# Optimization experiments

Measured on AMD Instinct MI355X. Metric: run time of the kernel, lower is better.

Reference implementation:

```python
import jax, jax.numpy as jnp
import numpy as np

N = 10000   # num nodes
E = 160000  # num edges (avg degree 16)
B = 8       # batch dim carried on node state
D = 64      # hidden_size


def setup_inputs() -> dict:
    key = jax.random.key(0)
    k1, k2, k3, k4, k5, k6 = jax.random.split(key, 6)
    state = jax.random.normal(k1, (N, B, D), jnp.float32)
    feature = jax.random.normal(k2, (N, 32), jnp.float32)  # unused by GAT math, kept for call signature
    weight = jax.random.normal(k3, (2 * D, D), jnp.float32) * 0.05
    src = jax.random.randint(k4, (E,), 0, N, jnp.int32)
    dst = jax.random.randint(k5, (E,), 0, N, jnp.int32)
    dist = jax.random.uniform(k6, (E, 1), jnp.float32)
    return dict(state=state, feature=feature, weight=weight, src=src, dst=dst, dist=dist)


def reference(state, feature, weight, src, dst, dist):
    # --- msg_edge: gather src/dst node states per edge ---
    src_state = state[src]                 # [E,B,D]
    dst_state = state[dst]                 # [E,B,D]
    es = jnp.concatenate([src_state, dst_state], axis=-1)          # [E,B,2D]
    alpha = jax.nn.leaky_relu(jnp.einsum('ebk,kd->ebd', es, weight),
                              negative_slope=0.2)                  # tf.nn.leaky_relu alpha=0.2
    alpha = alpha * dist[:, :, None]       # dist [E,1] broadcast to [E,1,1]

    # --- msg_reduce: segment softmax over incoming edges of each dst node ---
    amax = jax.ops.segment_max(alpha, dst, num_segments=N)         # [N,B,D]
    ex = jnp.exp(alpha - amax[dst])                                # stable exp
    denom = jax.ops.segment_sum(ex, dst, num_segments=N)           # [N,B,D]
    attn = ex / denom[dst]                                         # [E,B,D]

    # weighted sum of src states scattered back to dst nodes, then relu
    new_state = jax.nn.relu(jax.ops.segment_sum(attn * src_state, dst, num_segments=N))
    return new_state
```

## Files before the change

kernel.cpp:

```cpp
#include <hip/hip_runtime.h>
#include <hip/hip_fp16.h>
#include <math.h>

#define N_NODES 10000
#define N_EDGES 160000
#define B_ 8
#define D_ 64
#define BD 512
#define ROWS 80000
#define SLICE 640000
#define CAP 48
#define CAPR 56

typedef _Float16 f16x8 __attribute__((ext_vector_type(8)));
typedef float f32x4 __attribute__((ext_vector_type(4)));
typedef float f4v __attribute__((ext_vector_type(4)));
typedef unsigned int u32;

union HU { _Float16 f; unsigned short u; };
union HC { u32 u; __half2 h; };

__global__ void __launch_bounds__(256, 4) prep_kernel(
    const int* __restrict__ src, const int* __restrict__ dst,
    const float* __restrict__ dist, int* __restrict__ counts, u32* __restrict__ bucket,
    const float* __restrict__ state, const float* __restrict__ weight,
    u32* __restrict__ G, __half* __restrict__ Pd) {
    __shared__ _Float16 At[64 * 72];
    __shared__ char smemB[128 * 72 * 2];
    _Float16* Bt = (_Float16*)smemB;
    unsigned short* Ps2 = (unsigned short*)smemB;
    unsigned short* Ps  = (unsigned short*)(smemB + 8704);
    int bid = blockIdx.x;
    int tid = threadIdx.x;

    int s_e, d_e; float di_e;
    bool do_edge = tid < 128;
    if (do_edge) {
        int e = bid * 128 + tid;
        s_e = src[e];
        d_e = dst[e];
        di_e = dist[e];
    }

    int row0 = bid * 64;
    int wave = tid >> 6, lane = tid & 63;
    int quad = lane >> 4, m16 = lane & 15;
    int m_loc = wave * 16 + m16;

    const f4v* st4 = (const f4v*)(state + (size_t)row0 * 64);
    for (int i = tid; i < 1024; i += 256) {
        int r = i >> 4, c4 = (i & 15) << 2;
        f4v v = __builtin_nontemporal_load(&st4[i]);
        union { short4 s; _Float16 h[4]; } u;
        u.h[0] = (_Float16)v[0]; u.h[1] = (_Float16)v[1];
        u.h[2] = (_Float16)v[2]; u.h[3] = (_Float16)v[3];
        *(short4*)&At[r * 72 + c4] = u.s;
    }
    const f4v* w4 = (const f4v*)weight;
    for (int i = tid; i < 2048; i += 256) {
        int r = i >> 4, c4 = (i & 15) << 2;
        f4v v = w4[i];
        int h = r >> 6, k = r & 63;
        int nb = h * 64 + c4;
        Bt[(nb + 0) * 72 + k] = (_Float16)v[0];
        Bt[(nb + 1) * 72 + k] = (_Float16)v[1];
        Bt[(nb + 2) * 72 + k] = (_Float16)v[2];
        Bt[(nb + 3) * 72 + k] = (_Float16)v[3];
    }

    if (do_edge) {
        int pos = atomicAdd(&counts[d_e], 1);
        if (pos < CAP) {
            unsigned short hd = __half_as_ushort(__float2half_rn(di_e * 1.44269504f));
            bucket[d_e * CAPR + pos] = (u32)s_e | ((u32)hd << 16);
        }
    }
    __syncthreads();

    f16x8 bf0[8], bf1[8];
#pragma unroll
    for (int tcol = 0; tcol < 8; tcol++) {
        int n = tcol * 16 + m16;
        bf0[tcol] = *(const f16x8*)&Bt[n * 72 + quad * 8];
        bf1[tcol] = *(const f16x8*)&Bt[n * 72 + 32 + quad * 8];
    }
    f16x8 a0 = *(const f16x8*)&At[m_loc * 72 + quad * 8];
    f16x8 a1 = *(const f16x8*)&At[m_loc * 72 + 32 + quad * 8];
    __syncthreads();

#pragma unroll
    for (int tcol = 0; tcol < 8; tcol++) {
        int n = tcol * 16 + m16;
        f32x4 acc = {0.f, 0.f, 0.f, 0.f};
        acc = __builtin_amdgcn_mfma_f32_16x16x32_f16(a0, bf0[tcol], acc, 0, 0, 0);
        acc = __builtin_amdgcn_mfma_f32_16x16x32_f16(a1, bf1[tcol], acc, 0, 0, 0);
#pragma unroll
        for (int r = 0; r < 4; r++) {
            int ml = wave * 16 + quad * 4 + r;
            unsigned short ph = __half_as_ushort(__float2half_rn(acc[r]));
            if (tcol < 4) Ps2[ml * 68 + n] = ph;
            else          Ps[ml * 64 + (n - 64)] = ph;
        }
    }
    __syncthreads();

    const u32* Ps2w = (const u32*)Ps2;
    const u32* Atw = (const u32*)At;
    for (int i = tid; i < 1024; i += 256) {
        int row = i >> 4, q = i & 15;
        int m = row0 + row;
        size_t base = (size_t)(m & 7) * SLICE + (size_t)(m >> 3) * 64;
        u32 p01 = Ps2w[row * 34 + q * 2];
        u32 p23 = Ps2w[row * 34 + q * 2 + 1];
        u32 x01 = Atw[row * 36 + q * 2];
        u32 x23 = Atw[row * 36 + q * 2 + 1];
        float4 v = make_float4(__uint_as_float(p01), __uint_as_float(p23),
                               __uint_as_float(x01), __uint_as_float(x23));
        *(float4*)&G[base + q * 4] = v;
    }
    for (int i = tid; i < 512; i += 256) {
        int row = i >> 3, seg = i & 7;
        int m = row0 + row;
        size_t base = (size_t)(m & 7) * SLICE + (size_t)(m >> 3) * 64;
        *(float4*)&Pd[base + seg * 8] = *(const float4*)&Ps[row * 64 + seg * 8];
    }
}

__global__ void __launch_bounds__(256) gat_aggregate(
    const u32* __restrict__ G,
    const __half* __restrict__ Pds,
    const int* __restrict__ counts,
    const u32* __restrict__ bucket,
    float* __restrict__ out) {
    int bid = blockIdx.x;
    int b = bid & 7;
    int grp = bid >> 3;
    int wave = threadIdx.x >> 6;
    int lane = threadIdx.x & 63;
    int n0 = (grp << 3) + (wave << 1);
    int n1 = n0 + 1;
    int eidx = lane >> 4;
    int lpart = lane & 15;

    const u32* Gb = G + (size_t)b * SLICE;
    const __half* Pb = Pds + (size_t)b * SLICE;

    int cnt0 = counts[n0]; if (cnt0 > CAP) cnt0 = CAP;
    int cnt1 = counts[n1]; if (cnt1 > CAP) cnt1 = CAP;
    const u32* ep0 = bucket + n0 * CAPR;
    const u32* ep1 = bucket + n1 * CAPR;

    union { double d; __half2 h[2]; } pdu0, pdu1;
    pdu0.d = *(const double*)(Pb + n0 * 64 + lpart * 4);
    pdu1.d = *(const double*)(Pb + n1 * 64 + lpart * 4);

    u32 rA0 = ep0[eidx], rB0 = ep0[4 + eidx];
    u32 rA1 = ep1[eidx], rB1 = ep1[4 + eidx];
    float4 gA0 = *(const float4*)(Gb + (size_t)(rA0 & 0xffffu) * 64 + lpart * 4);
    float4 gB0 = *(const float4*)(Gb + (size_t)(rB0 & 0xffffu) * 64 + lpart * 4);
    float4 gA1 = *(const float4*)(Gb + (size_t)(rA1 & 0xffffu) * 64 + lpart * 4);
    float4 gB1 = *(const float4*)(Gb + (size_t)(rB1 & 0xffffu) * 64 + lpart * 4);
    __half hh;
    hh = __ushort_as_half((unsigned short)(rA0 >> 16)); __half2 dA0 = __halves2half2(hh, hh);
    hh = __ushort_as_half((unsigned short)(rB0 >> 16)); __half2 dB0 = __halves2half2(hh, hh);
    hh = __ushort_as_half((unsigned short)(rA1 >> 16)); __half2 dA1 = __halves2half2(hh, hh);
    hh = __ushort_as_half((unsigned short)(rB1 >> 16)); __half2 dB1 = __halves2half2(hh, hh);

    const __half2 c06 = __float2half2_rn(0.6f);
    const __half2 c04 = __float2half2_rn(0.4f);

    auto edge_body = [&](float4 g, __half2 dd, __half2 pd01, __half2 pd23,
                         __half2& l01, __half2& l23, __half2& o01, __half2& o23) {
        union { float4 f; __half2 h[4]; } gu; gu.f = g;
        __half2 z01 = __hadd2(gu.h[0], pd01);
        __half2 z23 = __hadd2(gu.h[1], pd23);
        HC zz01, zz23, az01, az23;
        zz01.h = z01; zz23.h = z23;
        az01.u = zz01.u & 0x7fff7fffu;
        az23.u = zz23.u & 0x7fff7fffu;
        __half2 lk01 = __hfma2(az01.h, c04, __hmul2(z01, c06));
        __half2 lk23 = __hfma2(az23.h, c04, __hmul2(z23, c06));
        __half2 a01 = __hmul2(lk01, dd);
        __half2 a23 = __hmul2(lk23, dd);
        __half2 e01 = __halves2half2(hexp2(__low2half(a01)), hexp2(__high2half(a01)));
        __half2 e23 = __halves2half2(hexp2(__low2half(a23)), hexp2(__high2half(a23)));
        l01 = __hadd2(l01, e01);
        l23 = __hadd2(l23, e23);
        o01 = __hfma2(e01, gu.h[2], o01);
        o23 = __hfma2(e23, gu.h[3], o23);
    };

    auto run_task = [&](const u32* ep, int cnt, __half2 pd01, __half2 pd23,
                        float4 gA, float4 gB, __half2 dA, __half2 dB,
                        __half2& l01, __half2& l23, __half2& o01, __half2& o23) {
        int padded4 = (cnt + 3) & ~3;
        int full8 = padded4 & ~7;
        if (full8 > 0) {
            int j = 0;
            for (;;) {
                int jn = j + 8;
                bool more = jn < full8;
                float4 gA2, gB2; __half2 dA2, dB2;
                if (more) {
                    u32 rA2 = ep[jn + eidx];
                    u32 rB2 = ep[jn + 4 + eidx];
                    gA2 = *(const float4*)(Gb + (size_t)(rA2 & 0xffffu) * 64 + lpart * 4);
                    gB2 = *(const float4*)(Gb + (size_t)(rB2 & 0xffffu) * 64 + lpart * 4);
                    __half h2a = __ushort_as_half((unsigned short)(rA2 >> 16));
                    __half h2b = __ushort_as_half((unsigned short)(rB2 >> 16));
                    dA2 = __halves2half2(h2a, h2a);
                    dB2 = __halves2half2(h2b, h2b);
                }
                edge_body(gA, dA, pd01, pd23, l01, l23, o01, o23);
                edge_body(gB, dB, pd01, pd23, l01, l23, o01, o23);
                if (!more) break;
                j = jn; gA = gA2; gB = gB2; dA = dA2; dB = dB2;
            }
            if (padded4 > full8) {
                u32 rec = ep[full8 + eidx];
                float4 g = *(const float4*)(Gb + (size_t)(rec & 0xffffu) * 64 + lpart * 4);
                __half hd = __ushort_as_half((unsigned short)(rec >> 16));
                edge_body(g, __halves2half2(hd, hd), pd01, pd23, l01, l23, o01, o23);
            }
        } else if (padded4 > 0) {
            edge_body(gA, dA, pd01, pd23, l01, l23, o01, o23);
        }
    };

    __half2 zero = __float2half2_rn(0.f);
    __half2 l01a = zero, l23a = zero, o01a = zero, o23a = zero;
    __half2 l01b = zero, l23b = zero, o01b = zero, o23b = zero;

    run_task(ep0, cnt0, pdu0.h[0], pdu0.h[1], gA0, gB0, dA0, dB0, l01a, l23a, o01a, o23a);
    run_task(ep1, cnt1, pdu1.h[0], pdu1.h[1], gA1, gB1, dA1, dB1, l01b, l23b, o01b, o23b);

    float4 g0 = *(const float4*)(Gb + lpart * 4);
    union { float4 f; __half2 h[4]; } g0u; g0u.f = g0;

    auto finish = [&](int cnt, __half2& l01, __half2& l23, __half2& o01, __half2& o23) {
        if (cnt <= 0) return;
#pragma unroll
        for (int m = 16; m <= 32; m <<= 1) {
            HC c;
            c.u = (u32)__shfl_xor((int)((HC){.h = l01}).u, m, 64); l01 = __hadd2(l01, c.h);
            c.u = (u32)__shfl_xor((int)((HC){.h = l23}).u, m, 64); l23 = __hadd2(l23, c.h);
            c.u = (u32)__shfl_xor((int)((HC){.h = o01}).u, m, 64); o01 = __hadd2(o01, c.h);
            c.u = (u32)__shfl_xor((int)((HC){.h = o23}).u, m, 64); o23 = __hadd2(o23, c.h);
        }
        int npads = ((cnt + 3) & ~3) - cnt;
        if (npads) {
            __half2 np = __float2half2_rn((float)npads);
            l01 = __hsub2(l01, np);
            l23 = __hsub2(l23, np);
            __half2 nneg = __hneg2(np);
            o01 = __hfma2(nneg, g0u.h[2], o01);
            o23 = __hfma2(nneg, g0u.h[3], o23);
        }
    };
    finish(cnt0, l01a, l23a, o01a, o23a);
    finish(cnt1, l01b, l23b, o01b, o23b);

    if (eidx == 0) {
        auto emit = [&](int n, int cnt, __half2 l01, __half2 l23, __half2 o01, __half2 o23) {
            float4 r;
            if (cnt > 0) {
                float l0 = __low2float(l01), l1 = __high2float(l01);
                float l2 = __low2float(l23), l3 = __high2float(l23);
                float o0 = __low2float(o01), o1 = __high2float(o01);
                float o2 = __low2float(o23), o3 = __high2float(o23);
                r.x = fmaxf(o0 * __builtin_amdgcn_rcpf(l0), 0.f);
                r.y = fmaxf(o1 * __builtin_amdgcn_rcpf(l1), 0.f);
                r.z = fmaxf(o2 * __builtin_amdgcn_rcpf(l2), 0.f);
                r.w = fmaxf(o3 * __builtin_amdgcn_rcpf(l3), 0.f);
            } else {
                r = make_float4(0.f, 0.f, 0.f, 0.f);
            }
            *(float4*)(out + (size_t)n * BD + b * 64 + lpart * 4) = r;
        };
        emit(n0, cnt0, l01a, l23a, o01a, o23a);
        emit(n1, cnt1, l01b, l23b, o01b, o23b);
    }
}

extern "C" void kernel_launch(void* const* d_in, const int* in_sizes, int n_in,
                              void* d_out, int out_size, void* d_ws, size_t ws_size,
                              hipStream_t stream) {
    const float* state  = (const float*)d_in[0];
    const float* weight = (const float*)d_in[2];
    const int*   src    = (const int*)d_in[3];
    const int*   dst    = (const int*)d_in[4];
    const float* dist   = (const float*)d_in[5];

    u32*    G      = (u32*)d_ws;
    __half* Pd     = (__half*)(G + (size_t)8 * SLICE);
    u32*    bucket = (u32*)(Pd + (size_t)8 * SLICE);
    int*    counts = (int*)(bucket + (size_t)N_NODES * CAPR);

    hipMemsetAsync(bucket, 0, ((size_t)N_NODES * CAPR + N_NODES) * sizeof(u32), stream);
    prep_kernel<<<1250, 256, 0, stream>>>(src, dst, dist, counts, bucket,
                                          state, weight, G, Pd);
    gat_aggregate<<<N_NODES, 256, 0, stream>>>(G, Pd, counts, bucket, (float*)d_out);
}
```

Baseline: 136.5 us.

## Use persistent blocks with atomic work queue per batch slice in aggregation

New measurement: 170.3 us. 24.8% more time.

```diff
diff --git a/kernel.cpp b/kernel.cpp
--- a/kernel.cpp
+++ b/kernel.cpp
@@ -7,10 +7,10 @@
 #define B_ 8
 #define D_ 64
 #define BD 512
-#define ROWS 80000
 #define SLICE 640000
 #define CAP 48
 #define CAPR 56
+#define NPAIRS 5000
 
 typedef _Float16 f16x8 __attribute__((ext_vector_type(8)));
 typedef float f32x4 __attribute__((ext_vector_type(4)));
@@ -131,43 +131,23 @@
     const __half* __restrict__ Pds,
     const int* __restrict__ counts,
     const u32* __restrict__ bucket,
+    int* __restrict__ q,
     float* __restrict__ out) {
-    int bid = blockIdx.x;
-    int b = bid & 7;
-    int grp = bid >> 3;
-    int wave = threadIdx.x >> 6;
+    int s = blockIdx.x & 7;
     int lane = threadIdx.x & 63;
-    int n0 = (grp << 3) + (wave << 1);
-    int n1 = n0 + 1;
     int eidx = lane >> 4;
     int lpart = lane & 15;
 
-    const u32* Gb = G + (size_t)b * SLICE;
-    const __half* Pb = Pds + (size_t)b * SLICE;
-
-    int cnt0 = counts[n0]; if (cnt0 > CAP) cnt0 = CAP;
-    int cnt1 = counts[n1]; if (cnt1 > CAP) cnt1 = CAP;
-    const u32* ep0 = bucket + n0 * CAPR;
-    const u32* ep1 = bucket + n1 * CAPR;
-
-    union { double d; __half2 h[2]; } pdu0, pdu1;
-    pdu0.d = *(const double*)(Pb + n0 * 64 + lpart * 4);
-    pdu1.d = *(const double*)(Pb + n1 * 64 + lpart * 4);
-
-    u32 rA0 = ep0[eidx], rB0 = ep0[4 + eidx];
-    u32 rA1 = ep1[eidx], rB1 = ep1[4 + eidx];
-    float4 gA0 = *(const float4*)(Gb + (size_t)(rA0 & 0xffffu) * 64 + lpart * 4);
-    float4 gB0 = *(const float4*)(Gb + (size_t)(rB0 & 0xffffu) * 64 + lpart * 4);
-    float4 gA1 = *(const float4*)(Gb + (size_t)(rA1 & 0xffffu) * 64 + lpart * 4);
-    float4 gB1 = *(const float4*)(Gb + (size_t)(rB1 & 0xffffu) * 64 + lpart * 4);
-    __half hh;
-    hh = __ushort_as_half((unsigned short)(rA0 >> 16)); __half2 dA0 = __halves2half2(hh, hh);
-    hh = __ushort_as_half((unsigned short)(rB0 >> 16)); __half2 dB0 = __halves2half2(hh, hh);
-    hh = __ushort_as_half((unsigned short)(rA1 >> 16)); __half2 dA1 = __halves2half2(hh, hh);
-    hh = __ushort_as_half((unsigned short)(rB1 >> 16)); __half2 dB1 = __halves2half2(hh, hh);
+    const u32* Gb = G + (size_t)s * SLICE;
+    const __half* Pb = Pds + (size_t)s * SLICE;
+    int* qs = q + s * 32;
 
     const __half2 c06 = __float2half2_rn(0.6f);
     const __half2 c04 = __float2half2_rn(0.4f);
+    const __half2 zero = __float2half2_rn(0.f);
+
+    float4 g0 = *(const float4*)(Gb + lpart * 4);
+    union { float4 f; __half2 h[4]; } g0u; g0u.f = g0;
 
     auto edge_body = [&](float4 g, __half2 dd, __half2 pd01, __half2 pd23,
                          __half2& l01, __half2& l23, __half2& o01, __half2& o23) {
@@ -227,16 +207,6 @@
         }
     };
 
-    __half2 zero = __float2half2_rn(0.f);
-    __half2 l01a = zero, l23a = zero, o01a = zero, o23a = zero;
-    __half2 l01b = zero, l23b = zero, o01b = zero, o23b = zero;
-
-    run_task(ep0, cnt0, pdu0.h[0], pdu0.h[1], gA0, gB0, dA0, dB0, l01a, l23a, o01a, o23a);
-    run_task(ep1, cnt1, pdu1.h[0], pdu1.h[1], gA1, gB1, dA1, dB1, l01b, l23b, o01b, o23b);
-
-    float4 g0 = *(const float4*)(Gb + lpart * 4);
-    union { float4 f; __half2 h[4]; } g0u; g0u.f = g0;
-
     auto finish = [&](int cnt, __half2& l01, __half2& l23, __half2& o01, __half2& o23) {
         if (cnt <= 0) return;
 #pragma unroll
@@ -257,28 +227,72 @@
             o23 = __hfma2(nneg, g0u.h[3], o23);
         }
     };
-    finish(cnt0, l01a, l23a, o01a, o23a);
-    finish(cnt1, l01b, l23b, o01b, o23b);
-
-    if (eidx == 0) {
-        auto emit = [&](int n, int cnt, __half2 l01, __half2 l23, __half2 o01, __half2 o23) {
-            float4 r;
-            if (cnt > 0) {
-                float l0 = __low2float(l01), l1 = __high2float(l01);
-                float l2 = __low2float(l23), l3 = __high2float(l23);
-                float o0 = __low2float(o01), o1 = __high2float(o01);
-                float o2 = __low2float(o23), o3 = __high2float(o23);
-                r.x = fmaxf(o0 * __builtin_amdgcn_rcpf(l0), 0.f);
-                r.y = fmaxf(o1 * __builtin_amdgcn_rcpf(l1), 0.f);
-                r.z = fmaxf(o2 * __builtin_amdgcn_rcpf(l2), 0.f);
-                r.w = fmaxf(o3 * __builtin_amdgcn_rcpf(l3), 0.f);
-            } else {
-                r = make_float4(0.f, 0.f, 0.f, 0.f);
-            }
-            *(float4*)(out + (size_t)n * BD + b * 64 + lpart * 4) = r;
-        };
-        emit(n0, cnt0, l01a, l23a, o01a, o23a);
-        emit(n1, cnt1, l01b, l23b, o01b, o23b);
+
+    auto do_pair = [&](int n0) {
+        int n1 = n0 + 1;
+        int2 c01 = *(const int2*)(counts + n0);
+        int cnt0 = c01.x > CAP ? CAP : c01.x;
+        int cnt1 = c01.y > CAP ? CAP : c01.y;
+        const u32* ep0 = bucket + n0 * CAPR;
+        const u32* ep1 = bucket + n1 * CAPR;
+
+        union { double d; __half2 h[2]; } pdu0, pdu1;
+        pdu0.d = *(const double*)(Pb + n0 * 64 + lpart * 4);
+        pdu1.d = *(const double*)(Pb + n1 * 64 + lpart * 4);
+
+        u32 rA0 = ep0[eidx], rB0 = ep0[4 + eidx];
+        u32 rA1 = ep1[eidx], rB1 = ep1[4 + eidx];
+        float4 gA0 = *(const float4*)(Gb + (size_t)(rA0 & 0xffffu) * 64 + lpart * 4);
+        float4 gB0 = *(const float4*)(Gb + (size_t)(rB0 & 0xffffu) * 64 + lpart * 4);
+        float4 gA1 = *(const float4*)(Gb + (size_t)(rA1 & 0xffffu) * 64 + lpart * 4);
+        float4 gB1 = *(const float4*)(Gb + (size_t)(rB1 & 0xffffu) * 64 + lpart * 4);
+        __half hh;
+        hh = __ushort_as_half((unsigned short)(rA0 >> 16)); __half2 dA0 = __halves2half2(hh, hh);
+        hh = __ushort_as_half((unsigned short)(rB0 >> 16)); __half2 dB0 = __halves2half2(hh, hh);
+        hh = __ushort_as_half((unsigned short)(rA1 >> 16)); __half2 dA1 = __halves2half2(hh, hh);
+        hh = __ushort_as_half((unsigned short)(rB1 >> 16)); __half2 dB1 = __halves2half2(hh, hh);
+
+        __half2 l01a = zero, l23a = zero, o01a = zero, o23a = zero;
+        __half2 l01b = zero, l23b = zero, o01b = zero, o23b = zero;
+
+        run_task(ep0, cnt0, pdu0.h[0], pdu0.h[1], gA0, gB0, dA0, dB0, l01a, l23a, o01a, o23a);
+        run_task(ep1, cnt1, pdu1.h[0], pdu1.h[1], gA1, gB1, dA1, dB1, l01b, l23b, o01b, o23b);
+
+        finish(cnt0, l01a, l23a, o01a, o23a);
+        finish(cnt1, l01b, l23b, o01b, o23b);
+
+        if (eidx == 0) {
+            auto emit = [&](int n, int cnt, __half2 l01, __half2 l23, __half2 o01, __half2 o23) {
+                float4 r;
+                if (cnt > 0) {
+                    float l0 = __low2float(l01), l1 = __high2float(l01);
+                    float l2 = __low2float(l23), l3 = __high2float(l23);
+                    float o0 = __low2float(o01), o1 = __high2float(o01);
+                    float o2 = __low2float(o23), o3 = __high2float(o23);
+                    r.x = fmaxf(o0 * __builtin_amdgcn_rcpf(l0), 0.f);
+                    r.y = fmaxf(o1 * __builtin_amdgcn_rcpf(l1), 0.f);
+                    r.z = fmaxf(o2 * __builtin_amdgcn_rcpf(l2), 0.f);
+                    r.w = fmaxf(o3 * __builtin_amdgcn_rcpf(l3), 0.f);
+                } else {
+                    r = make_float4(0.f, 0.f, 0.f, 0.f);
+                }
+                *(float4*)(out + (size_t)n * BD + s * 64 + lpart * 4) = r;
+            };
+            emit(n0, cnt0, l01a, l23a, o01a, o23a);
+            emit(n1, cnt1, l01b, l23b, o01b, o23b);
+        }
+    };
+
+    int tv = 0;
+    if (lane == 0) tv = atomicAdd(qs, 2);
+    int t = __shfl(tv, 0, 64);
+    while (t < NPAIRS) {
+        int tnv = 0;
+        if (lane == 0) tnv = atomicAdd(qs, 2);
+        int tn = __shfl(tnv, 0, 64);
+        do_pair(2 * t);
+        if (t + 1 < NPAIRS) do_pair(2 * (t + 1));
+        t = tn;
     }
 }
 
@@ -295,9 +309,10 @@
     __half* Pd     = (__half*)(G + (size_t)8 * SLICE);
     u32*    bucket = (u32*)(Pd + (size_t)8 * SLICE);
     int*    counts = (int*)(bucket + (size_t)N_NODES * CAPR);
-
-    hipMemsetAsync(bucket, 0, ((size_t)N_NODES * CAPR + N_NODES) * sizeof(u32), stream);
+    int*    q      = counts + N_NODES;
+
+    hipMemsetAsync(bucket, 0, ((size_t)N_NODES * CAPR + N_NODES + 256) * sizeof(u32), stream);
     prep_kernel<<<1250, 256, 0, stream>>>(src, dst, dist, counts, bucket,
                                           state, weight, G, Pd);
-    gat_aggregate<<<N_NODES, 256, 0, stream>>>(G, Pd, counts, bucket, (float*)d_out);
+    gat_aggregate<<<2048, 256, 0, stream>>>(G, Pd, counts, bucket, q, (float*)d_out);
 }
```
